# Kernel optimization log

Measured on AMD Instinct MI355X. Metric: run time of the kernel, lower is better.

## Reference

```python
import jax, jax.numpy as jnp
import numpy as np

NUM_CLASSES = 200
NPC = 10  # prototypes per class
P = NUM_CLASSES * NPC
D = 128


def setup_inputs() -> dict:
    key = jax.random.key(0)
    kx, kp = jax.random.split(key)
    x = jax.random.normal(kx, (16, D, 56, 56), dtype=jnp.float32)
    prototypes = jax.random.normal(kp, (1, P, D), dtype=jnp.float32)
    return {"x": x, "prototypes": prototypes}


def _cdist(a, b):
    # a: [B, N, D], b: [1, P, D] -> [B, N, P] Euclidean distances
    a2 = jnp.sum(a * a, axis=-1, keepdims=True)            # [B, N, 1]
    b2 = jnp.sum(b * b, axis=-1)[:, None, :]               # [1, 1, P]
    ab = jnp.einsum('bnd,zpd->bnp', a, b)                  # [B, N, P]
    d2 = jnp.maximum(a2 + b2 - 2.0 * ab, 0.0)
    return jnp.sqrt(d2)


def reference(x, prototypes):
    B, C, H, W = x.shape
    xf = x.reshape(B, C, H * W).transpose(0, 2, 1)         # [B, N, D]
    distances = _cdist(xf, prototypes)                     # [B, N, P]
    similarity = jnp.log((distances + 1.0) / (distances + 1e-7))
    max_similarity = jnp.max(similarity, axis=1)           # [B, P]
    min_distances = jnp.min(distances, axis=1)             # [B, P]
    arg_min = jnp.argmin(distances, axis=1)                # [B, P]
    min_features = jnp.take_along_axis(xf, arg_min[:, :, None], axis=1)  # [B, P, D]
    min_distances_per_class = min_distances.reshape(B, NUM_CLASSES, NPC)
    return (max_similarity, min_distances_per_class, min_features)
```

## Files before the change

### kernel.cpp

```cpp
#include <hip/hip_runtime.h>
#include <hip/hip_bf16.h>
#include <cmath>

#define DDIM 128
#define NPTS 3136
#define NCHUNK 196
#define QCHUNK 49
#define BATCH 16
#define PROT 2000
#define PPAD 2048

typedef __attribute__((ext_vector_type(8))) short bf16x8;
typedef __attribute__((ext_vector_type(4))) float f32x4;
typedef __attribute__((ext_vector_type(4))) unsigned int u32x4;

#define WS_X2   0
#define WS_K1   50176
#define WS_K2   181248
#define WS_PT   312320
#define WS_XT   443392
#define WS_XFT  3654656
#define WS_MID  ((size_t)3654656 * 4)
#define WS_BIG  ((size_t)10077184 * 4)

__device__ inline unsigned short bf16rn(float a) {
    unsigned u = __float_as_uint(a);
    unsigned r = u + 0x7FFFu + ((u >> 16) & 1u);
    return (unsigned short)(r >> 16);
}

__device__ __forceinline__ void gload_lds16(const void* g, void* l) {
    __builtin_amdgcn_global_load_lds(
        (const __attribute__((address_space(1))) void*)g,
        (__attribute__((address_space(3))) void*)l, 16, 0, 0);
}
__device__ __forceinline__ void gload_lds4(const void* g, void* l) {
    __builtin_amdgcn_global_load_lds(
        (const __attribute__((address_space(1))) void*)g,
        (__attribute__((address_space(3))) void*)l, 4, 0, 0);
}

__global__ __launch_bounds__(256)
void pp_fused(const float* __restrict__ x, const float* __restrict__ proto,
              unsigned short* __restrict__ xt, unsigned short* __restrict__ pt,
              float* __restrict__ x2, float* __restrict__ xfT) {
    int tid = threadIdx.x;
    if (blockIdx.x == 49) {
        int by = blockIdx.y;
        if (by >= 8) return;
        int p = by * 256 + tid;
        int ps = min(p, PROT - 1);
        const float* src = proto + (size_t)ps * DDIM;
        unsigned short* dst = pt + (size_t)p * 128;
        for (int j = 0; j < DDIM; ++j) dst[j] = bf16rn(src[j]);
        return;
    }
    __shared__ float xs[DDIM][64];
    int b = blockIdx.y;
    int n0 = blockIdx.x * 64;
    {
        int r = tid >> 4, c = tid & 15;
        #pragma unroll
        for (int it = 0; it < 8; ++it) {
            int row = it * 16 + r;
            f32x4 v = *(const f32x4*)(x + ((size_t)(b * DDIM + row)) * NPTS + n0 + c * 4);
            *(f32x4*)(&xs[row][c * 4]) = v;
        }
    }
    __syncthreads();
    if (tid < 64) {
        float s = 0.f;
        #pragma unroll 8
        for (int d = 0; d < DDIM; ++d) { float v = xs[d][tid]; s = fmaf(v, v, s); }
        x2[b * NPTS + n0 + tid] = (s + 512.0f) * 512.0f;
    }
    int n = tid & 63, kk = tid >> 6;
    int nl = n & 15, ci = (n0 + n) >> 4;
    unsigned int hw[16];
    #pragma unroll
    for (int j = 0; j < 16; ++j) {
        unsigned short h0 = bf16rn(xs[kk * 32 + 2 * j][n]);
        unsigned short h1 = bf16rn(xs[kk * 32 + 2 * j + 1][n]);
        hw[j] = (unsigned)h0 | ((unsigned)h1 << 16);
    }
    char* cb = (char*)xt + ((size_t)b * NCHUNK + ci) * 4096;
    #pragma unroll
    for (int g = 0; g < 4; ++g)
        *(u32x4*)(cb + kk * 1024 + g * 256 + nl * 16) = *(u32x4*)(&hw[g * 4]);
    if (xfT) {
        float* fo = xfT + ((size_t)b * NPTS + n0 + n) * DDIM + kk * 32;
        #pragma unroll
        for (int g = 0; g < 8; ++g) {
            f32x4 v;
            v[0] = xs[kk * 32 + g * 4 + 0][n];
            v[1] = xs[kk * 32 + g * 4 + 1][n];
            v[2] = xs[kk * 32 + g * 4 + 2][n];
            v[3] = xs[kk * 32 + g * 4 + 3][n];
            *(f32x4*)(fo + g * 4) = v;
        }
    }
}

__global__ __launch_bounds__(256, 8)
void proto_mfma(const unsigned short* __restrict__ xt,
                const unsigned short* __restrict__ pt,
                const float* __restrict__ x2,
                unsigned* __restrict__ k1w, unsigned* __restrict__ k2w) {
    __shared__ __align__(16) char LDS[20480];
    float* x2s = (float*)LDS;
    char*  AsB = LDS + 4096;

    int lid = blockIdx.x;
    int sid = (lid & 7) * 256 + (lid >> 3);
    int b = sid >> 7;
    int rest = sid & 127;
    int pbase = (rest >> 2) * 64;
    int q = rest & 3;

    int tid = threadIdx.x;
    int lane = tid & 63, psg = tid >> 6;
    int l15 = lane & 15, lg = lane >> 4;

    const unsigned short* bp = pt + (size_t)(pbase + psg * 16 + l15) * 128 + lg * 8;
    bf16x8 B0 = *(const bf16x8*)(bp);
    bf16x8 B1 = *(const bf16x8*)(bp + 32);
    bf16x8 B2 = *(const bf16x8*)(bp + 64);
    bf16x8 B3 = *(const bf16x8*)(bp + 96);

    const char* srcBase = (const char*)xt + ((size_t)b * NCHUNK + q * QCHUNK) * 4096;
    const char* aread = AsB + lane * 16;
    const int qOfs = q * (QCHUNK * 16);
    const int nbBase = qOfs + lg * 4;

    unsigned K1 = 0xFFFFFFFFu, K2 = 0xFFFFFFFFu;

    {
        const float* xsrc = x2 + (size_t)b * NPTS + qOfs;
        #pragma unroll
        for (int r = 0; r < 4; ++r)
            gload_lds4(xsrc + min(r * 256 + psg * 64 + lane, QCHUNK * 16 - 1),
                       (char*)x2s + (r * 256 + psg * 64) * 4);
    }
    #pragma unroll
    for (int r = 0; r < 3; ++r)
        gload_lds16(srcBase + (size_t)r * 4096 + psg * 1024 + (size_t)lane * 16,
                    AsB + r * 4096 + psg * 1024);

#define PMF_BODY(T, U)                                                              \
    {                                                                               \
        asm volatile("s_waitcnt vmcnt(2)" ::: "memory");                            \
        __builtin_amdgcn_s_barrier();                                               \
        int cln = (T) + 3;                                                          \
        cln = cln > QCHUNK - 1 ? QCHUNK - 1 : cln;                                  \
        gload_lds16(srcBase + (size_t)cln * 4096 + psg * 1024 + (size_t)lane * 16,  \
                    AsB + (((U) + 3) & 3) * 4096 + psg * 1024);                     \
        f32x4 xv = *(const f32x4*)&x2s[(T) * 16 + lg * 4];                          \
        const char* ar = aread + (U) * 4096;                                        \
        f32x4 acc = {0.f, 0.f, 0.f, 0.f};                                           \
        __builtin_amdgcn_s_setprio(1);                                              \
        acc = __builtin_amdgcn_mfma_f32_16x16x32_bf16(*(const bf16x8*)(ar),        B0, acc, 0, 0, 0); \
        acc = __builtin_amdgcn_mfma_f32_16x16x32_bf16(*(const bf16x8*)(ar + 1024), B1, acc, 0, 0, 0); \
        acc = __builtin_amdgcn_mfma_f32_16x16x32_bf16(*(const bf16x8*)(ar + 2048), B2, acc, 0, 0, 0); \
        acc = __builtin_amdgcn_mfma_f32_16x16x32_bf16(*(const bf16x8*)(ar + 3072), B3, acc, 0, 0, 0); \
        __builtin_amdgcn_s_setprio(0);                                              \
        int nb = nbBase + (T) * 16;                                                 \
        _Pragma("unroll")                                                           \
        for (int rr = 0; rr < 4; ++rr) {                                            \
            float f = fmaf(acc[rr], -1024.f, xv[rr]);                               \
            unsigned k = ((unsigned)f << 12) | (unsigned)(nb + rr);                 \
            K2 = min(K2, max(K1, k));                                               \
            K1 = min(K1, k);                                                        \
        }                                                                           \
    }

    #pragma unroll 1
    for (int t0 = 0; t0 < 48; t0 += 4) {
        PMF_BODY(t0 + 0, 0)
        PMF_BODY(t0 + 1, 1)
        PMF_BODY(t0 + 2, 2)
        PMF_BODY(t0 + 3, 3)
    }
    PMF_BODY(48, 0)
#undef PMF_BODY

    #pragma unroll
    for (int m = 16; m <= 32; m <<= 1) {
        unsigned c1 = (unsigned)__shfl_xor((int)K1, m, 64);
        unsigned c2 = (unsigned)__shfl_xor((int)K2, m, 64);
        unsigned w  = max(K1, c1);
        K1 = min(K1, c1);
        K2 = min(w, min(K2, c2));
    }
    if (lg == 0) {
        size_t o = ((size_t)b * 4 + q) * PPAD + pbase + psg * 16 + l15;
        k1w[o] = K1;
        k2w[o] = K2;
    }
}

template<int MODE>
__global__ __launch_bounds__(256)
void fixup(const float* __restrict__ x, const float* __restrict__ xfT,
           const float* __restrict__ proto,
           const unsigned* __restrict__ k1w, const unsigned* __restrict__ k2w,
           float* __restrict__ out) {
    int tid = threadIdx.x;
    int lane = tid & 63, wv = tid >> 6;
    long long pair = (long long)blockIdx.x * 4 + wv;
    if (pair >= (long long)BATCH * PROT) return;
    int b = (int)(pair / PROT), p = (int)(pair % PROT);
    unsigned a0 = k1w[((size_t)b * 4 + 0) * PPAD + p];
    unsigned a1 = k1w[((size_t)b * 4 + 1) * PPAD + p];
    unsigned a2 = k1w[((size_t)b * 4 + 2) * PPAD + p];
    unsigned a3 = k1w[((size_t)b * 4 + 3) * PPAD + p];
    unsigned c0 = k2w[((size_t)b * 4 + 0) * PPAD + p];
    unsigned c1 = k2w[((size_t)b * 4 + 1) * PPAD + p];
    unsigned c2 = k2w[((size_t)b * 4 + 2) * PPAD + p];
    unsigned c3 = k2w[((size_t)b * 4 + 3) * PPAD + p];
    int cand[4];
    cand[0] = (int)(min(a0, a1) & 0xFFFu);
    cand[1] = (int)(min(max(a0, a1), min(c0, c1)) & 0xFFFu);
    cand[2] = (int)(min(a2, a3) & 0xFFFu);
    cand[3] = (int)(min(max(a2, a3), min(c2, c3)) & 0xFFFu);

    int d0 = lane, d1 = lane + 64;
    float pa0 = proto[(size_t)p * DDIM + d0], pa1 = proto[(size_t)p * DDIM + d1];
    float sp2 = pa0 * pa0 + pa1 * pa1;
    float f0[4], f1[4], sxp[4], sx2[4];
    #pragma unroll
    for (int c = 0; c < 4; ++c) {
        int n = cand[c];
        float v0, v1;
        if (MODE == 0) {
            const float* f = xfT + ((size_t)b * NPTS + n) * DDIM;
            v0 = f[d0]; v1 = f[d1];
        } else {
            const float* xb = x + (size_t)b * DDIM * NPTS;
            v0 = xb[(size_t)d0 * NPTS + n]; v1 = xb[(size_t)d1 * NPTS + n];
        }
        f0[c] = v0; f1[c] = v1;
        sxp[c] = v0 * pa0 + v1 * pa1;
        sx2[c] = v0 * v0 + v1 * v1;
    }
    #pragma unroll
    for (int m = 1; m < 64; m <<= 1) {
        sp2 += __shfl_xor(sp2, m, 64);
        #pragma unroll
        for (int c = 0; c < 4; ++c) {
            sxp[c] += __shfl_xor(sxp[c], m, 64);
            sx2[c] += __shfl_xor(sx2[c], m, 64);
        }
    }
    float bd = 3e38f; int bn = 0x7FFFFFFF; int bc = 0;
    #pragma unroll
    for (int c = 0; c < 4; ++c) {
        float d2 = fmaxf(sx2[c] + sp2 - 2.f * sxp[c], 0.f);
        bool w = (d2 < bd) || (d2 == bd && cand[c] < bn);
        bd = w ? d2 : bd;
        bn = w ? cand[c] : bn;
        bc = w ? c : bc;
    }
    float dm = sqrtf(bd);
    float sim = logf((dm + 1.0f) / (dm + 1e-7f));
    if (lane == 0) {
        out[(size_t)b * PROT + p] = sim;
        out[(size_t)BATCH * PROT + (size_t)b * PROT + p] = dm;
    }
    float o0 = f0[0], o1 = f1[0];
    #pragma unroll
    for (int c = 1; c < 4; ++c) {
        o0 = (bc == c) ? f0[c] : o0;
        o1 = (bc == c) ? f1[c] : o1;
    }
    float* fo = out + (size_t)2 * BATCH * PROT + ((size_t)b * PROT + p) * DDIM;
    fo[d0] = o0;
    fo[d1] = o1;
}

#define TP 64
#define TN 64
__global__ void p2_kernel(const float* __restrict__ proto, float* __restrict__ p2) {
    int p = blockIdx.x * blockDim.x + threadIdx.x;
    if (p >= PROT) return;
    const float4* pr = reinterpret_cast<const float4*>(proto + (size_t)p * DDIM);
    float s = 0.f;
    #pragma unroll
    for (int i = 0; i < DDIM / 4; ++i) {
        float4 v = pr[i];
        s += v.x * v.x + v.y * v.y + v.z * v.z + v.w * v.w;
    }
    p2[p] = s;
}
__global__ void x2_kernel(const float* __restrict__ x, float* __restrict__ x2) {
    int idx = blockIdx.x * blockDim.x + threadIdx.x;
    if (idx >= BATCH * NPTS) return;
    int b = idx / NPTS, n = idx - b * NPTS;
    const float* xp = x + (size_t)b * DDIM * NPTS + n;
    float s = 0.f;
    #pragma unroll 8
    for (int d = 0; d < DDIM; ++d) { float v = xp[(size_t)d * NPTS]; s += v * v; }
    x2[idx] = s;
}
__global__ __launch_bounds__(256, 2)
void proto_main(const float* __restrict__ x, const float* __restrict__ proto,
                const float* __restrict__ p2, const float* __restrict__ x2,
                float* __restrict__ out) {
    __shared__ __align__(16) float xs[DDIM][TN];
    __shared__ __align__(16) float pst[DDIM][TP];
    __shared__ float p2s[TP];
    __shared__ float x2s[TN];
    __shared__ float red_d2[16][TP];
    __shared__ int   red_n[16][TP];
    __shared__ int   bestn_s[TP];
    const int b = blockIdx.y;
    const int pbase = blockIdx.x * TP;
    const int tid = threadIdx.x;
    {
        #pragma unroll
        for (int it = 0; it < (TP * DDIM / 4) / 256; ++it) {
            int idx = it * 256 + tid;
            int p = idx / (DDIM / 4);
            int dq = idx - p * (DDIM / 4);
            int gp = min(pbase + p, PROT - 1);
            float4 v = reinterpret_cast<const float4*>(proto)[(size_t)gp * (DDIM / 4) + dq];
            pst[dq * 4 + 0][p] = v.x; pst[dq * 4 + 1][p] = v.y;
            pst[dq * 4 + 2][p] = v.z; pst[dq * 4 + 3][p] = v.w;
        }
        if (tid < TP) p2s[tid] = p2[min(pbase + tid, PROT - 1)];
    }
    const int tn = tid >> 4;
    const int tp = tid & 15;
    float best[4]; int bestn[4];
    #pragma unroll
    for (int j = 0; j < 4; ++j) { best[j] = 1e30f; bestn[j] = 0; }
    for (int n0 = 0; n0 < NPTS; n0 += TN) {
        __syncthreads();
        {
            int r = tid >> 4, c = tid & 15;
            #pragma unroll
            for (int it = 0; it < 8; ++it) {
                int row = it * 16 + r;
                float4 v = *reinterpret_cast<const float4*>(
                    x + ((size_t)(b * DDIM + row)) * NPTS + n0 + c * 4);
                *reinterpret_cast<float4*>(&xs[row][c * 4]) = v;
            }
        }
        if (tid < TN) x2s[tid] = x2[b * NPTS + n0 + tid];
        __syncthreads();
        float acc[4][4];
        #pragma unroll
        for (int i = 0; i < 4; ++i)
            #pragma unroll
            for (int j = 0; j < 4; ++j) acc[i][j] = 0.f;
        #pragma unroll 16
        for (int d = 0; d < DDIM; ++d) {
            const float4 a = *reinterpret_cast<const float4*>(&xs[d][tn * 4]);
            const float4 bv = *reinterpret_cast<const float4*>(&pst[d][tp * 4]);
            const float av[4] = {a.x, a.y, a.z, a.w};
            const float bw[4] = {bv.x, bv.y, bv.z, bv.w};
            #pragma unroll
            for (int i = 0; i < 4; ++i)
                #pragma unroll
                for (int j = 0; j < 4; ++j) acc[i][j] = fmaf(av[i], bw[j], acc[i][j]);
        }
        #pragma unroll
        for (int i = 0; i < 4; ++i) {
            float xv = x2s[tn * 4 + i];
            int n = n0 + tn * 4 + i;
            #pragma unroll
            for (int j = 0; j < 4; ++j) {
                float d2 = xv + p2s[tp * 4 + j] - 2.0f * acc[i][j];
                if (d2 < best[j]) { best[j] = d2; bestn[j] = n; }
            }
        }
    }
    #pragma unroll
    for (int j = 0; j < 4; ++j) {
        red_d2[tn][tp * 4 + j] = best[j];
        red_n[tn][tp * 4 + j] = bestn[j];
    }
    __syncthreads();
    if (tid < TP) {
        float bd = red_d2[0][tid]; int bn = red_n[0][tid];
        #pragma unroll
        for (int t = 1; t < 16; ++t) {
            float dv = red_d2[t][tid]; int nv = red_n[t][tid];
            if (dv < bd || (dv == bd && nv < bn)) { bd = dv; bn = nv; }
        }
        int gp = pbase + tid;
        if (gp < PROT) {
            float d2c = fmaxf(bd, 0.f);
            float dmin = sqrtf(d2c);
            float sim = logf((dmin + 1.0f) / (dmin + 1e-7f));
            out[(size_t)b * PROT + gp] = sim;
            out[(size_t)BATCH * PROT + (size_t)b * PROT + gp] = dmin;
        }
        bestn_s[tid] = bn;
    }
    __syncthreads();
    {
        int pl = tid >> 2, dbase = (tid & 3) * 32;
        int gp = pbase + pl;
        if (gp < PROT) {
            int n = bestn_s[pl];
            float* dst = out + (size_t)2 * BATCH * PROT + ((size_t)(b * PROT + gp)) * DDIM + dbase;
            const float* src = x + ((size_t)(b * DDIM + dbase)) * NPTS + n;
            #pragma unroll 8
            for (int d = 0; d < 32; ++d) dst[d] = src[(size_t)d * NPTS];
        }
    }
}

extern "C" void kernel_launch(void* const* d_in, const int* in_sizes, int n_in,
                              void* d_out, int out_size, void* d_ws, size_t ws_size,
                              hipStream_t stream) {
    const float* x = (const float*)d_in[0];
    const float* proto = (const float*)d_in[1];
    float* out = (float*)d_out;
    float* ws = (float*)d_ws;

    if (ws_size >= WS_MID) {
        bool big = (ws_size >= WS_BIG);
        float* x2 = ws + WS_X2;
        unsigned* k1w = (unsigned*)(ws + WS_K1);
        unsigned* k2w = (unsigned*)(ws + WS_K2);
        unsigned short* pt = (unsigned short*)(ws + WS_PT);
        unsigned short* xt = (unsigned short*)(ws + WS_XT);
        float* xfT = big ? (ws + WS_XFT) : nullptr;

        pp_fused<<<dim3(50, BATCH), 256, 0, stream>>>(x, proto, xt, pt, x2, xfT);
        proto_mfma<<<2048, 256, 0, stream>>>(xt, pt, x2, k1w, k2w);
        if (big)
            fixup<0><<<(BATCH * PROT) / 4, 256, 0, stream>>>(x, xfT, proto, k1w, k2w, out);
        else
            fixup<1><<<(BATCH * PROT) / 4, 256, 0, stream>>>(x, nullptr, proto, k1w, k2w, out);
    } else {
        float* p2 = ws;
        float* x2 = ws + 2048;
        p2_kernel<<<(PROT + 255) / 256, 256, 0, stream>>>(proto, p2);
        x2_kernel<<<(BATCH * NPTS + 255) / 256, 256, 0, stream>>>(x, x2);
        dim3 grid((PROT + TP - 1) / TP, BATCH);
        proto_main<<<grid, 256, 0, stream>>>(x, proto, p2, x2, out);
    }
}
```

Measured before the change: 81.72 us.

## Double prototypes per wave in MFMA distance kernel to reuse A fragments

Each wave now handles 32 prototypes instead of 16, holding two sets of B fragments in registers. Each A fragment loaded from LDS feeds two interleaved MFMA chains, which halves how often the staged x tiles are re-read per prototype. The grid shrinks from 2048 to 1024 blocks, and the launch bound drops to 4 waves per EU to allow the extra registers. The cost is lower occupancy and fewer blocks to hide the load pipeline.

```diff
diff --git a/kernel.cpp b/kernel.cpp
--- a/kernel.cpp
+++ b/kernel.cpp
@@ -101,7 +101,7 @@
     }
 }
 
-__global__ __launch_bounds__(256, 8)
+__global__ __launch_bounds__(256, 4)
 void proto_mfma(const unsigned short* __restrict__ xt,
                 const unsigned short* __restrict__ pt,
                 const float* __restrict__ x2,
@@ -111,28 +111,34 @@
     char*  AsB = LDS + 4096;
 
     int lid = blockIdx.x;
-    int sid = (lid & 7) * 256 + (lid >> 3);
-    int b = sid >> 7;
-    int rest = sid & 127;
-    int pbase = (rest >> 2) * 64;
+    int sid = (lid & 7) * 128 + (lid >> 3);
+    int b = sid >> 6;
+    int rest = sid & 63;
+    int pbase = (rest >> 2) * 128;
     int q = rest & 3;
 
     int tid = threadIdx.x;
     int lane = tid & 63, psg = tid >> 6;
     int l15 = lane & 15, lg = lane >> 4;
 
-    const unsigned short* bp = pt + (size_t)(pbase + psg * 16 + l15) * 128 + lg * 8;
-    bf16x8 B0 = *(const bf16x8*)(bp);
-    bf16x8 B1 = *(const bf16x8*)(bp + 32);
-    bf16x8 B2 = *(const bf16x8*)(bp + 64);
-    bf16x8 B3 = *(const bf16x8*)(bp + 96);
+    const unsigned short* bpa = pt + (size_t)(pbase + psg * 32 + l15) * 128 + lg * 8;
+    const unsigned short* bpb = bpa + (size_t)16 * 128;
+    bf16x8 Ba0 = *(const bf16x8*)(bpa);
+    bf16x8 Ba1 = *(const bf16x8*)(bpa + 32);
+    bf16x8 Ba2 = *(const bf16x8*)(bpa + 64);
+    bf16x8 Ba3 = *(const bf16x8*)(bpa + 96);
+    bf16x8 Bb0 = *(const bf16x8*)(bpb);
+    bf16x8 Bb1 = *(const bf16x8*)(bpb + 32);
+    bf16x8 Bb2 = *(const bf16x8*)(bpb + 64);
+    bf16x8 Bb3 = *(const bf16x8*)(bpb + 96);
 
     const char* srcBase = (const char*)xt + ((size_t)b * NCHUNK + q * QCHUNK) * 4096;
     const char* aread = AsB + lane * 16;
     const int qOfs = q * (QCHUNK * 16);
     const int nbBase = qOfs + lg * 4;
 
-    unsigned K1 = 0xFFFFFFFFu, K2 = 0xFFFFFFFFu;
+    unsigned K1a = 0xFFFFFFFFu, K2a = 0xFFFFFFFFu;
+    unsigned K1b = 0xFFFFFFFFu, K2b = 0xFFFFFFFFu;
 
     {
         const float* xsrc = x2 + (size_t)b * NPTS + qOfs;
@@ -145,6 +151,15 @@
     for (int r = 0; r < 3; ++r)
         gload_lds16(srcBase + (size_t)r * 4096 + psg * 1024 + (size_t)lane * 16,
                     AsB + r * 4096 + psg * 1024);
+
+#define PMF_TRACK(ACC, XV, NB, K1, K2)                                              \
+        _Pragma("unroll")                                                           \
+        for (int rr = 0; rr < 4; ++rr) {                                            \
+            float f = fmaf((ACC)[rr], -1024.f, (XV)[rr]);                           \
+            unsigned k = ((unsigned)f << 12) | (unsigned)((NB) + rr);               \
+            K2 = min(K2, max(K1, k));                                               \
+            K1 = min(K1, k);                                                        \
+        }
 
 #define PMF_BODY(T, U)                                                              \
     {                                                                               \
@@ -156,21 +171,25 @@
                     AsB + (((U) + 3) & 3) * 4096 + psg * 1024);                     \
         f32x4 xv = *(const f32x4*)&x2s[(T) * 16 + lg * 4];                          \
         const char* ar = aread + (U) * 4096;                                        \
-        f32x4 acc = {0.f, 0.f, 0.f, 0.f};                                           \
+        bf16x8 A0 = *(const bf16x8*)(ar);                                           \
+        bf16x8 A1 = *(const bf16x8*)(ar + 1024);                                    \
+        bf16x8 A2 = *(const bf16x8*)(ar + 2048);                                    \
+        bf16x8 A3 = *(const bf16x8*)(ar + 3072);                                    \
+        f32x4 accA = {0.f, 0.f, 0.f, 0.f};                                          \
+        f32x4 accB = {0.f, 0.f, 0.f, 0.f};                                          \
         __builtin_amdgcn_s_setprio(1);                                              \
-        acc = __builtin_amdgcn_mfma_f32_16x16x32_bf16(*(const bf16x8*)(ar),        B0, acc, 0, 0, 0); \
-        acc = __builtin_amdgcn_mfma_f32_16x16x32_bf16(*(const bf16x8*)(ar + 1024), B1, acc, 0, 0, 0); \
-        acc = __builtin_amdgcn_mfma_f32_16x16x32_bf16(*(const bf16x8*)(ar + 2048), B2, acc, 0, 0, 0); \
-        acc = __builtin_amdgcn_mfma_f32_16x16x32_bf16(*(const bf16x8*)(ar + 3072), B3, acc, 0, 0, 0); \
+        accA = __builtin_amdgcn_mfma_f32_16x16x32_bf16(A0, Ba0, accA, 0, 0, 0);     \
+        accB = __builtin_amdgcn_mfma_f32_16x16x32_bf16(A0, Bb0, accB, 0, 0, 0);     \
+        accA = __builtin_amdgcn_mfma_f32_16x16x32_bf16(A1, Ba1, accA, 0, 0, 0);     \
+        accB = __builtin_amdgcn_mfma_f32_16x16x32_bf16(A1, Bb1, accB, 0, 0, 0);     \
+        accA = __builtin_amdgcn_mfma_f32_16x16x32_bf16(A2, Ba2, accA, 0, 0, 0);     \
+        accB = __builtin_amdgcn_mfma_f32_16x16x32_bf16(A2, Bb2, accB, 0, 0, 0);     \
+        accA = __builtin_amdgcn_mfma_f32_16x16x32_bf16(A3, Ba3, accA, 0, 0, 0);     \
+        accB = __builtin_amdgcn_mfma_f32_16x16x32_bf16(A3, Bb3, accB, 0, 0, 0);     \
         __builtin_amdgcn_s_setprio(0);                                              \
         int nb = nbBase + (T) * 16;                                                 \
-        _Pragma("unroll")                                                           \
-        for (int rr = 0; rr < 4; ++rr) {                                            \
-            float f = fmaf(acc[rr], -1024.f, xv[rr]);                               \
-            unsigned k = ((unsigned)f << 12) | (unsigned)(nb + rr);                 \
-            K2 = min(K2, max(K1, k));                                               \
-            K1 = min(K1, k);                                                        \
-        }                                                                           \
+        PMF_TRACK(accA, xv, nb, K1a, K2a)                                           \
+        PMF_TRACK(accB, xv, nb, K1b, K2b)                                           \
     }
 
     #pragma unroll 1
@@ -182,19 +201,27 @@
     }
     PMF_BODY(48, 0)
 #undef PMF_BODY
+#undef PMF_TRACK
 
     #pragma unroll
     for (int m = 16; m <= 32; m <<= 1) {
-        unsigned c1 = (unsigned)__shfl_xor((int)K1, m, 64);
-        unsigned c2 = (unsigned)__shfl_xor((int)K2, m, 64);
-        unsigned w  = max(K1, c1);
-        K1 = min(K1, c1);
-        K2 = min(w, min(K2, c2));
+        unsigned c1a = (unsigned)__shfl_xor((int)K1a, m, 64);
+        unsigned c2a = (unsigned)__shfl_xor((int)K2a, m, 64);
+        unsigned wa  = max(K1a, c1a);
+        K1a = min(K1a, c1a);
+        K2a = min(wa, min(K2a, c2a));
+        unsigned c1b = (unsigned)__shfl_xor((int)K1b, m, 64);
+        unsigned c2b = (unsigned)__shfl_xor((int)K2b, m, 64);
+        unsigned wb  = max(K1b, c1b);
+        K1b = min(K1b, c1b);
+        K2b = min(wb, min(K2b, c2b));
     }
     if (lg == 0) {
-        size_t o = ((size_t)b * 4 + q) * PPAD + pbase + psg * 16 + l15;
-        k1w[o] = K1;
-        k2w[o] = K2;
+        size_t o = ((size_t)b * 4 + q) * PPAD + pbase + psg * 32 + l15;
+        k1w[o] = K1a;
+        k2w[o] = K2a;
+        k1w[o + 16] = K1b;
+        k2w[o + 16] = K2b;
     }
 }
 
@@ -429,7 +456,7 @@
         float* xfT = big ? (ws + WS_XFT) : nullptr;
 
         pp_fused<<<dim3(50, BATCH), 256, 0, stream>>>(x, proto, xt, pt, x2, xfT);
-        proto_mfma<<<2048, 256, 0, stream>>>(xt, pt, x2, k1w, k2w);
+        proto_mfma<<<1024, 256, 0, stream>>>(xt, pt, x2, k1w, k2w);
         if (big)
             fixup<0><<<(BATCH * PROT) / 4, 256, 0, stream>>>(x, xfT, proto, k1w, k2w, out);
         else
```

Measured after the change: 78.44 us. 1.04x faster.
